# Kernel tuning notes

Hardware: AMD Instinct MI355X
Metric: run time of the kernel (lower is better)

## Reference

```python
import jax, jax.numpy as jnp
import numpy as np

EPS = 1e-5

def _conv1x1(x, w, b):
    # x: (b,c,h,w), w: (o,c) -> (b,o,h,w)
    return jnp.einsum('bchw,oc->bohw', x, w) + b[None, :, None, None]

def _maxpool2(x):
    b, c, h, w = x.shape
    return x.reshape(b, c, h // 2, 2, w // 2, 2).max(axis=(3, 5))

def setup_inputs() -> dict:
    key = jax.random.key(0)
    ks = jax.random.split(key, 11)
    C, CI, H, W, B = 256, 128, 64, 64, 8
    s = 0.05
    return {
        'x': jax.random.normal(ks[0], (B, C, H, W), jnp.float32),
        'Wg': jax.random.normal(ks[1], (CI, C), jnp.float32) * s,
        'bg': jax.random.normal(ks[2], (CI,), jnp.float32) * s,
        'Wt': jax.random.normal(ks[3], (CI, C), jnp.float32) * s,
        'bt': jax.random.normal(ks[4], (CI,), jnp.float32) * s,
        'Wp': jax.random.normal(ks[5], (CI, C), jnp.float32) * s,
        'bp': jax.random.normal(ks[6], (CI,), jnp.float32) * s,
        'Ww': jax.random.normal(ks[7], (C, CI), jnp.float32) * s,
        'bw': jax.random.normal(ks[8], (C,), jnp.float32) * s,
        'gamma': jax.random.normal(ks[9], (C,), jnp.float32),
        'beta': jax.random.normal(ks[10], (C,), jnp.float32),
    }

def reference(x, Wg, bg, Wt, bt, Wp, bp, Ww, bw, gamma, beta):
    b, C, H, W = x.shape
    CI = Wg.shape[0]
    # g and phi are sub-sampled by 2x2 max pool -> M = (H/2)*(W/2); theta keeps N = H*W
    g_x = _maxpool2(_conv1x1(x, Wg, bg)).reshape(b, CI, -1).transpose(0, 2, 1)   # (b,M,ci)
    theta_x = _conv1x1(x, Wt, bt).reshape(b, CI, -1).transpose(0, 2, 1)          # (b,N,ci)
    phi_x = _maxpool2(_conv1x1(x, Wp, bp)).reshape(b, CI, -1)                    # (b,ci,M)
    f = jnp.einsum('bnc,bcm->bnm', theta_x, phi_x)                               # (b,N,M)
    f_div_C = jax.nn.softmax(f, axis=-1)
    y = jnp.einsum('bnm,bmc->bnc', f_div_C, g_x)                                 # (b,N,ci)
    y = y.transpose(0, 2, 1).reshape(b, CI, H, W)
    # W: 1x1 conv + BatchNorm2d (training mode: batch statistics, biased var)
    wy = _conv1x1(y, Ww, bw)
    mean = wy.mean(axis=(0, 2, 3), keepdims=True)
    var = ((wy - mean) ** 2).mean(axis=(0, 2, 3), keepdims=True)
    wy = (wy - mean) * jax.lax.rsqrt(var + EPS)
    wy = wy * gamma[None, :, None, None] + beta[None, :, None, None]
    z = wy + x
    # self.avg_pool is AdaptiveMaxPool2d(1): global spatial max
    return z.max(axis=(2, 3), keepdims=True)
```

## Files before the change

### kernel.cpp

```cpp
#include <hip/hip_runtime.h>
#include <hip/hip_bf16.h>
#include <stdint.h>

using f32x4  = __attribute__((ext_vector_type(4))) float;
using bf16x8 = __attribute__((ext_vector_type(8))) short;
using short4v = __attribute__((ext_vector_type(4))) short;

#define DEVINL static __device__ __forceinline__

DEVINL short f2bf(float f) {
    union { float f; uint32_t u; } v; v.f = f;
    uint32_t r = (v.u + 0x7FFFu + ((v.u >> 16) & 1u)) >> 16;
    return (short)(uint16_t)r;
}
DEVINL float bf2f(short s) {
    union { uint32_t u; float f; } v; v.u = ((uint32_t)(uint16_t)s) << 16;
    return v.f;
}
DEVINL float fexp2(float x) {
    float r;
    asm("v_exp_f32 %0, %1" : "=v"(r) : "v"(x));
    return r;
}

DEVINL void gld16(const short* g, short* l) {
    __builtin_amdgcn_global_load_lds(
        (const __attribute__((address_space(1))) unsigned int*)g,
        (__attribute__((address_space(3))) unsigned int*)l, 16, 0, 0);
}

#define LOG2E 1.44269504f

__global__ __launch_bounds__(256) void k0_prep(
        const float* __restrict__ Wg, const float* __restrict__ Wt, const float* __restrict__ Wp,
        const float* __restrict__ bg, const float* __restrict__ bt, const float* __restrict__ bp,
        const float* __restrict__ Ww,
        short* __restrict__ W_all, short* __restrict__ Ww16, float* __restrict__ b_all) {
    int i = blockIdx.x * 256 + threadIdx.x;
    if (i < 384 * 256) {
        int r = i >> 8, c = i & 255;
        float v = (r < 128) ? Wg[r * 256 + c]
                : (r < 256) ? Wt[(r - 128) * 256 + c] * LOG2E
                            : Wp[(r - 256) * 256 + c];
        W_all[i] = f2bf(v);
    } else if (i < 384 * 256 + 256 * 128) {
        int j = i - 384 * 256;
        Ww16[j] = f2bf(Ww[j]);
    }
    if (i < 384) {
        b_all[i] = (i < 128) ? bg[i] : (i < 256) ? bt[i - 128] * LOG2E : bp[i - 256];
    }
}

__global__ __launch_bounds__(256) void k1_conv(const float* __restrict__ x,
        const short* __restrict__ W_all, const float* __restrict__ b_all,
        short* __restrict__ OutT, short* __restrict__ Kmat, short* __restrict__ Vmat) {
    __shared__ short xs[128 * 32];
    __shared__ short obuf[128 * 128];
    const int ntile = blockIdx.x;
    const int otile = blockIdx.y;
    const int b     = blockIdx.z;
    const int tid  = threadIdx.x;
    const int lane = tid & 63;
    const int wave = tid >> 6;
    const int wn = wave >> 1, wo = wave & 1;
    const int l15 = lane & 15, lh = lane >> 4;

    f32x4 acc[4][4];
    #pragma unroll
    for (int i = 0; i < 4; i++)
        #pragma unroll
        for (int j = 0; j < 4; j++) acc[i][j] = f32x4{0.f, 0.f, 0.f, 0.f};

    const int n0 = ntile * 128;
    const int ob = otile * 128 + wo * 64;
    const float* xb = x + (size_t)b * 256 * 4096;

    const int srow_base = (lane & 15) + wave * 16;
    const int sc0 = (lane >> 4) * 8;

    for (int kt = 0; kt < 8; kt++) {
        __syncthreads();
        #pragma unroll
        for (int p = 0; p < 2; p++) {
            int row = srow_base + p * 64;
            const float* xp = xb + (size_t)(kt * 32 + sc0) * 4096 + n0 + row;
            bf16x8 w8;
            #pragma unroll
            for (int j = 0; j < 8; j++) w8[j] = f2bf(xp[(size_t)j * 4096]);
            int ch = (sc0 >> 3) ^ ((row >> 1) & 3);
            *(bf16x8*)&xs[row * 32 + ch * 8] = w8;
        }
        __syncthreads();

        bf16x8 a[4], w[4];
        #pragma unroll
        for (int nf = 0; nf < 4; nf++) {
            int row = wn * 64 + nf * 16 + l15;
            int ch  = lh ^ ((row >> 1) & 3);
            a[nf] = *(const bf16x8*)&xs[row * 32 + ch * 8];
        }
        #pragma unroll
        for (int of = 0; of < 4; of++)
            w[of] = *(const bf16x8*)(W_all + (size_t)(ob + of * 16 + l15) * 256 + kt * 32 + lh * 8);
        #pragma unroll
        for (int nf = 0; nf < 4; nf++)
            #pragma unroll
            for (int of = 0; of < 4; of++)
                acc[nf][of] = __builtin_amdgcn_mfma_f32_16x16x32_bf16(a[nf], w[of], acc[nf][of], 0, 0, 0);
    }

    #pragma unroll
    for (int of = 0; of < 4; of++) {
        int ocol = wo * 64 + of * 16 + l15;
        float bias = b_all[otile * 128 + ocol];
        #pragma unroll
        for (int nf = 0; nf < 4; nf++)
            #pragma unroll
            for (int r = 0; r < 4; r++) {
                int n  = wn * 64 + nf * 16 + lh * 4 + r;
                int ch = (ocol >> 3) ^ (n & 15);
                obuf[n * 128 + ch * 8 + (ocol & 7)] = f2bf(acc[nf][of][r] + bias);
            }
    }
    __syncthreads();

    if (otile == 1) {
        #pragma unroll
        for (int p = 0; p < 8; p++) {
            int n  = wave * 4 + lh + p * 16;
            int ch = l15 ^ (n & 15);
            bf16x8 v = *(const bf16x8*)&obuf[n * 128 + ch * 8];
            *(bf16x8*)(OutT + ((size_t)b * 4096 + n0 + n) * 128 + l15 * 8) = v;
        }
    } else if (otile == 2) {
        const int wp = tid >> 3;
        const int cc = (tid & 7) * 16;
        short* kdst = Kmat + ((size_t)b * 1024 + ntile * 32 + wp) * 128 + cc;
        #pragma unroll
        for (int cblk = 0; cblk < 2; cblk++) {
            const int chunk = (cc >> 3) + cblk;
            float mx[8];
            #pragma unroll
            for (int j = 0; j < 8; j++) mx[j] = -1e30f;
            #pragma unroll
            for (int q4 = 0; q4 < 4; q4++) {
                int n = (q4 >> 1) * 64 + 2 * wp + (q4 & 1);
                bf16x8 v = *(const bf16x8*)&obuf[n * 128 + ((chunk ^ (n & 15)) * 8)];
                #pragma unroll
                for (int j = 0; j < 8; j++) mx[j] = fmaxf(mx[j], bf2f(v[j]));
            }
            bf16x8 vo;
            #pragma unroll
            for (int j = 0; j < 8; j++) vo[j] = f2bf(mx[j]);
            *(bf16x8*)(kdst + cblk * 8) = vo;
        }
    } else {
        const int c   = tid >> 1;
        const int wp0 = (tid & 1) * 16;
        const int chb = c >> 3, cl = c & 7;
        #pragma unroll
        for (int half = 0; half < 2; half++) {
            bf16x8 vo;
            #pragma unroll
            for (int j = 0; j < 8; j++) {
                int wp = wp0 + half * 8 + j;
                float mx = -1e30f;
                #pragma unroll
                for (int q4 = 0; q4 < 4; q4++) {
                    int n = (q4 >> 1) * 64 + 2 * wp + (q4 & 1);
                    mx = fmaxf(mx, bf2f(obuf[n * 128 + ((chb ^ (n & 15)) * 8) + cl]));
                }
                vo[j] = f2bf(mx);
            }
            *(bf16x8*)(Vmat + ((size_t)b * 128 + c) * 1024 + ntile * 32 + wp0 + half * 8) = vo;
        }
    }
}

__global__ __launch_bounds__(256) void k3_attn(const short* __restrict__ OutT,
        const short* __restrict__ Kmat, const short* __restrict__ Vmat,
        const short* __restrict__ Ww16, const float* __restrict__ bw,
        short* __restrict__ wy) {
    __shared__ short smem[36864];
    short* const sKb = smem;
    short* const sVb = smem + 16384;
    short* const sPb = smem + 32768;

    const int bid = blockIdx.x;
    const int b   = bid & 7;
    const int nt  = bid >> 3;
    const int tid = threadIdx.x;
    const int lane = tid & 63;
    const int wave = tid >> 6;
    const int l15 = lane & 15, lh = lane >> 4;
    const int nblk = nt * 64;
    const int n0 = nblk + wave * 16;

    const short* Kb = Kmat + (size_t)b * 1024 * 128;
    const short* Vb = Vmat + (size_t)b * 128 * 1024;
    short* sPw = sPb + wave * 1024;

    auto STAGE = [&](int t, int bufi) {
        const int m0 = t * 64;
        #pragma unroll
        for (int i = 0; i < 4; i++) {
            const int segb = (i * 4 + wave) * 64;
            const int rowK = (segb >> 4) + (lane >> 4);
            const int chkK = lane & 15;
            gld16(Kb + (size_t)(m0 + rowK) * 128 + ((chkK ^ (rowK & 15)) << 3),
                  sKb + bufi * 8192 + segb * 8);
            const int rowV = (segb >> 3) + (lane >> 3);
            const int chkV = lane & 7;
            gld16(Vb + (size_t)rowV * 1024 + m0 + ((chkV ^ (rowV & 7)) << 3),
                  sVb + bufi * 8192 + segb * 8);
        }
    };

    bf16x8 q[4];
    {
        const short* qrow = OutT + ((size_t)b * 4096 + n0 + l15) * 128;
        #pragma unroll
        for (int ks = 0; ks < 4; ks++)
            q[ks] = *(const bf16x8*)(qrow + ks * 32 + lh * 8);
    }

    f32x4 y[8];
    #pragma unroll
    for (int cf = 0; cf < 8; cf++) y[cf] = f32x4{0.f, 0.f, 0.f, 0.f};
    float mrun = -1e30f, lrun = 0.f;

    STAGE(0, 0);
    int cur = 0;

    for (int t = 0; t < 16; t++) {
        if (t < 15) {
            STAGE(t + 1, cur ^ 1);
            asm volatile("s_waitcnt vmcnt(8)" ::: "memory");
        } else {
            asm volatile("s_waitcnt vmcnt(0)" ::: "memory");
        }
        __builtin_amdgcn_s_barrier();
        __builtin_amdgcn_sched_barrier(0);

        const short* cK = sKb + cur * 8192;
        const short* cV = sVb + cur * 8192;

        f32x4 S[4];
        #pragma unroll
        for (int mf = 0; mf < 4; mf++) S[mf] = f32x4{0.f, 0.f, 0.f, 0.f};
        #pragma unroll
        for (int ks = 0; ks < 4; ks++) {
            bf16x8 kf[4];
            #pragma unroll
            for (int mf = 0; mf < 4; mf++) {
                int mrow = mf * 16 + l15;
                int jj   = ks * 4 + lh;
                kf[mf] = *(const bf16x8*)&cK[mrow * 128 + ((jj ^ (mrow & 15)) << 3)];
            }
            __builtin_amdgcn_s_setprio(1);
            #pragma unroll
            for (int mf = 0; mf < 4; mf++)
                S[mf] = __builtin_amdgcn_mfma_f32_16x16x32_bf16(kf[mf], q[ks], S[mf], 0, 0, 0);
            __builtin_amdgcn_s_setprio(0);
        }

        float pm = S[0][0];
        #pragma unroll
        for (int mf = 0; mf < 4; mf++)
            #pragma unroll
            for (int r = 0; r < 4; r++) pm = fmaxf(pm, S[mf][r]);
        pm = fmaxf(pm, __shfl_xor(pm, 16));
        pm = fmaxf(pm, __shfl_xor(pm, 32));

        if (__any(pm > mrun + 8.656f)) {
            float mnew  = fmaxf(mrun, pm);
            float alpha = fexp2(mrun - mnew);
            mrun = mnew;
            lrun *= alpha;
            float aR[4];
            #pragma unroll
            for (int r = 0; r < 4; r++) aR[r] = __shfl(alpha, lh * 4 + r);
            #pragma unroll
            for (int cf = 0; cf < 8; cf++)
                #pragma unroll
                for (int r = 0; r < 4; r++) y[cf][r] *= aR[r];
        }
        float rs = 0.f;
        #pragma unroll
        for (int mf = 0; mf < 4; mf++)
            #pragma unroll
            for (int r = 0; r < 4; r++) {
                float p = fexp2(S[mf][r] - mrun);
                S[mf][r] = p;
                rs += p;
            }
        rs += __shfl_xor(rs, 16);
        rs += __shfl_xor(rs, 32);
        lrun += rs;

        #pragma unroll
        for (int mf = 0; mf < 4; mf++) {
            short4v pk = { f2bf(S[mf][0]), f2bf(S[mf][1]), f2bf(S[mf][2]), f2bf(S[mf][3]) };
            *(short4v*)&sPw[(l15 << 6) + (((mf * 4 + lh) ^ l15) << 2)] = pk;
        }

        #pragma unroll
        for (int ks2 = 0; ks2 < 2; ks2++) {
            int u0 = ks2 * 8 + lh * 2;
            short4v lo = *(const short4v*)&sPw[(l15 << 6) + (((u0)     ^ l15) << 2)];
            short4v hi = *(const short4v*)&sPw[(l15 << 6) + (((u0 + 1) ^ l15) << 2)];
            bf16x8 pa = { lo.x, lo.y, lo.z, lo.w, hi.x, hi.y, hi.z, hi.w };
            int jj = ks2 * 4 + lh;
            __builtin_amdgcn_s_setprio(1);
            #pragma unroll
            for (int cf = 0; cf < 8; cf++) {
                int crow = cf * 16 + l15;
                bf16x8 vf = *(const bf16x8*)&cV[crow * 64 + ((jj ^ (crow & 7)) << 3)];
                y[cf] = __builtin_amdgcn_mfma_f32_16x16x32_bf16(pa, vf, y[cf], 0, 0, 0);
            }
            __builtin_amdgcn_s_setprio(0);
        }

        __builtin_amdgcn_sched_barrier(0);
        __builtin_amdgcn_s_barrier();
        cur ^= 1;
    }

    float linv[4];
    #pragma unroll
    for (int r = 0; r < 4; r++) linv[r] = 1.f / __shfl(lrun, lh * 4 + r);

    short* const Yt = smem;
    #pragma unroll
    for (int cf = 0; cf < 8; cf++) {
        int c = cf * 16 + l15;
        #pragma unroll
        for (int r = 0; r < 4; r++) {
            int n = wave * 16 + lh * 4 + r;
            Yt[n * 128 + (((c >> 3) ^ (n & 15)) << 3) + (c & 7)] = f2bf(y[cf][r] * linv[r]);
        }
    }
    __syncthreads();

    bf16x8 by[4][4];
    #pragma unroll
    for (int nf = 0; nf < 4; nf++)
        #pragma unroll
        for (int ks = 0; ks < 4; ks++) {
            int n  = nf * 16 + l15;
            int kc = ks * 4 + lh;
            by[nf][ks] = *(const bf16x8*)&Yt[n * 128 + ((kc ^ (n & 15)) << 3)];
        }

    short* const sOut = smem + 8192 + wave * 4608;
    const int obase = wave * 64;
    #pragma unroll
    for (int of = 0; of < 4; of++) {
        bf16x8 aw[4];
        #pragma unroll
        for (int ks = 0; ks < 4; ks++)
            aw[ks] = *(const bf16x8*)(Ww16 + (size_t)(obase + of * 16 + l15) * 128 + ks * 32 + lh * 8);
        #pragma unroll
        for (int nf = 0; nf < 4; nf++) {
            f32x4 acc = f32x4{0.f, 0.f, 0.f, 0.f};
            #pragma unroll
            for (int ks = 0; ks < 4; ks++)
                acc = __builtin_amdgcn_mfma_f32_16x16x32_bf16(aw[ks], by[nf][ks], acc, 0, 0, 0);
            #pragma unroll
            for (int r = 0; r < 4; r++) {
                int o_loc = of * 16 + lh * 4 + r;
                sOut[o_loc * 72 + nf * 16 + l15] = f2bf(acc[r] + bw[obase + o_loc]);
            }
        }
    }

    #pragma unroll
    for (int p = 0; p < 8; p++) {
        int o_loc = p * 8 + (lane >> 3);
        int n8    = (lane & 7) * 8;
        bf16x8 v = *(const bf16x8*)&sOut[o_loc * 72 + n8];
        *(bf16x8*)(wy + ((size_t)b * 256 + obase + o_loc) * 4096 + nblk + n8) = v;
    }
}

__global__ __launch_bounds__(256) void k4s_stats(const short* __restrict__ wy,
        float* __restrict__ stats) {
    const int o = blockIdx.x;
    const int tid = threadIdx.x;
    float s = 0.f, s2 = 0.f;
    #pragma unroll
    for (int b = 0; b < 8; b++) {
        const short* p = wy + ((size_t)b * 256 + o) * 4096;
        #pragma unroll
        for (int i = 0; i < 2; i++) {
            bf16x8 v = *(const bf16x8*)(p + (tid + i * 256) * 8);
            #pragma unroll
            for (int j = 0; j < 8; j++) {
                float f = bf2f(v[j]);
                s += f; s2 += f * f;
            }
        }
    }
    #pragma unroll
    for (int off = 1; off < 64; off <<= 1) { s += __shfl_xor(s, off); s2 += __shfl_xor(s2, off); }
    __shared__ float red[4][2];
    if ((tid & 63) == 0) { red[tid >> 6][0] = s; red[tid >> 6][1] = s2; }
    __syncthreads();
    if (tid == 0) {
        stats[o * 2]     = red[0][0] + red[1][0] + red[2][0] + red[3][0];
        stats[o * 2 + 1] = red[0][1] + red[1][1] + red[2][1] + red[3][1];
    }
}

__global__ __launch_bounds__(256) void k5_bnmax(const short* __restrict__ wy,
        const float* __restrict__ x, const float* __restrict__ stats,
        const float* __restrict__ gamma, const float* __restrict__ beta,
        float* __restrict__ outp) {
    int b = blockIdx.x >> 8;
    int o = blockIdx.x & 255;
    int tid = threadIdx.x;
    float mean = stats[o * 2] * (1.f / 32768.f);
    float var  = stats[o * 2 + 1] * (1.f / 32768.f) - mean * mean;
    float rstd = rsqrtf(var + 1e-5f);
    float A = rstd * gamma[o];
    float B = beta[o] - mean * A;
    const short* pw = wy + ((size_t)b * 256 + o) * 4096;
    const float* px = x + ((size_t)b * 256 + o) * 4096;
    float mx = -1e30f;
    #pragma unroll
    for (int j = 0; j < 2; j++) {
        int e = (tid + j * 256) * 8;
        bf16x8 w8 = *(const bf16x8*)(pw + e);
        float4 xa = *(const float4*)(px + e);
        float4 xb = *(const float4*)(px + e + 4);
        mx = fmaxf(mx, bf2f(w8[0]) * A + B + xa.x);
        mx = fmaxf(mx, bf2f(w8[1]) * A + B + xa.y);
        mx = fmaxf(mx, bf2f(w8[2]) * A + B + xa.z);
        mx = fmaxf(mx, bf2f(w8[3]) * A + B + xa.w);
        mx = fmaxf(mx, bf2f(w8[4]) * A + B + xb.x);
        mx = fmaxf(mx, bf2f(w8[5]) * A + B + xb.y);
        mx = fmaxf(mx, bf2f(w8[6]) * A + B + xb.z);
        mx = fmaxf(mx, bf2f(w8[7]) * A + B + xb.w);
    }
    #pragma unroll
    for (int off = 1; off < 64; off <<= 1) mx = fmaxf(mx, __shfl_xor(mx, off));
    __shared__ float red[4];
    if ((tid & 63) == 0) red[tid >> 6] = mx;
    __syncthreads();
    if (tid == 0)
        outp[b * 256 + o] = fmaxf(fmaxf(red[0], red[1]), fmaxf(red[2], red[3]));
}

extern "C" void kernel_launch(void* const* d_in, const int* in_sizes, int n_in,
                              void* d_out, int out_size, void* d_ws, size_t ws_size,
                              hipStream_t stream) {
    const float* x     = (const float*)d_in[0];
    const float* Wg    = (const float*)d_in[1];
    const float* bg    = (const float*)d_in[2];
    const float* Wt    = (const float*)d_in[3];
    const float* bt    = (const float*)d_in[4];
    const float* Wp    = (const float*)d_in[5];
    const float* bp    = (const float*)d_in[6];
    const float* Ww    = (const float*)d_in[7];
    const float* bw    = (const float*)d_in[8];
    const float* gamma = (const float*)d_in[9];
    const float* beta  = (const float*)d_in[10];
    float* outp = (float*)d_out;

    char* ws = (char*)d_ws;
    size_t off = 0;
    auto alloc = [&](size_t bytes) -> void* {
        void* p = ws + off;
        off = (off + bytes + 255) & ~(size_t)255;
        return p;
    };
    short* W_all = (short*)alloc((size_t)384 * 256 * 2);
    short* Ww16  = (short*)alloc((size_t)256 * 128 * 2);
    float* b_all = (float*)alloc((size_t)384 * 4);
    short* OutT  = (short*)alloc((size_t)8 * 4096 * 128 * 2);
    short* Kmat  = (short*)alloc((size_t)8 * 1024 * 128 * 2);
    short* Vmat  = (short*)alloc((size_t)8 * 128 * 1024 * 2);
    short* wy    = (short*)alloc((size_t)8 * 256 * 4096 * 2);
    float* stats = (float*)alloc((size_t)256 * 2 * 4);

    k0_prep<<<512, 256, 0, stream>>>(Wg, Wt, Wp, bg, bt, bp, Ww, W_all, Ww16, b_all);
    k1_conv<<<dim3(32, 3, 8), 256, 0, stream>>>(x, W_all, b_all, OutT, Kmat, Vmat);
    k3_attn<<<512, 256, 0, stream>>>(OutT, Kmat, Vmat, Ww16, bw, wy);
    k4s_stats<<<256, 256, 0, stream>>>(wy, stats);
    k5_bnmax<<<2048, 256, 0, stream>>>(wy, x, stats, gamma, beta, outp);
}
```

Measured before the change: 88.93 us.

## Fuse BN statistics into attention epilogue and compute softmax row sums via MFMA

```diff
diff --git a/kernel.cpp b/kernel.cpp
--- a/kernel.cpp
+++ b/kernel.cpp
@@ -22,6 +22,11 @@
     asm("v_exp_f32 %0, %1" : "=v"(r) : "v"(x));
     return r;
 }
+DEVINL uint32_t cvtpk(float a, float b) {
+    uint32_t r;
+    asm("v_cvt_pk_bf16_f32 %0, %1, %2" : "=v"(r) : "v"(a), "v"(b));
+    return r;
+}
 
 DEVINL void gld16(const short* g, short* l) {
     __builtin_amdgcn_global_load_lds(
@@ -35,8 +40,13 @@
         const float* __restrict__ Wg, const float* __restrict__ Wt, const float* __restrict__ Wp,
         const float* __restrict__ bg, const float* __restrict__ bt, const float* __restrict__ bp,
         const float* __restrict__ Ww,
-        short* __restrict__ W_all, short* __restrict__ Ww16, float* __restrict__ b_all) {
+        short* __restrict__ W_all, short* __restrict__ Ww16, float* __restrict__ b_all,
+        float* __restrict__ stats) {
     int i = blockIdx.x * 256 + threadIdx.x;
+    if (blockIdx.x == 0) {
+        stats[threadIdx.x] = 0.f;
+        stats[threadIdx.x + 256] = 0.f;
+    }
     if (i < 384 * 256) {
         int r = i >> 8, c = i & 255;
         float v = (r < 128) ? Wg[r * 256 + c]
@@ -181,7 +191,7 @@
 __global__ __launch_bounds__(256) void k3_attn(const short* __restrict__ OutT,
         const short* __restrict__ Kmat, const short* __restrict__ Vmat,
         const short* __restrict__ Ww16, const float* __restrict__ bw,
-        short* __restrict__ wy) {
+        short* __restrict__ wy, float* __restrict__ stats) {
     __shared__ short smem[36864];
     short* const sKb = smem;
     short* const sVb = smem + 16384;
@@ -224,11 +234,15 @@
         for (int ks = 0; ks < 4; ks++)
             q[ks] = *(const bf16x8*)(qrow + ks * 32 + lh * 8);
     }
+    bf16x8 vone;
+    #pragma unroll
+    for (int j = 0; j < 8; j++) vone[j] = (short)0x3F80;
 
     f32x4 y[8];
     #pragma unroll
     for (int cf = 0; cf < 8; cf++) y[cf] = f32x4{0.f, 0.f, 0.f, 0.f};
-    float mrun = -1e30f, lrun = 0.f;
+    f32x4 ysum = f32x4{0.f, 0.f, 0.f, 0.f};
+    float mrun = -1e30f;
 
     STAGE(0, 0);
     int cur = 0;
@@ -277,7 +291,6 @@
             float mnew  = fmaxf(mrun, pm);
             float alpha = fexp2(mrun - mnew);
             mrun = mnew;
-            lrun *= alpha;
             float aR[4];
             #pragma unroll
             for (int r = 0; r < 4; r++) aR[r] = __shfl(alpha, lh * 4 + r);
@@ -285,24 +298,19 @@
             for (int cf = 0; cf < 8; cf++)
                 #pragma unroll
                 for (int r = 0; r < 4; r++) y[cf][r] *= aR[r];
-        }
-        float rs = 0.f;
+            #pragma unroll
+            for (int r = 0; r < 4; r++) ysum[r] *= aR[r];
+        }
         #pragma unroll
         for (int mf = 0; mf < 4; mf++)
             #pragma unroll
-            for (int r = 0; r < 4; r++) {
-                float p = fexp2(S[mf][r] - mrun);
-                S[mf][r] = p;
-                rs += p;
-            }
-        rs += __shfl_xor(rs, 16);
-        rs += __shfl_xor(rs, 32);
-        lrun += rs;
+            for (int r = 0; r < 4; r++)
+                S[mf][r] = fexp2(S[mf][r] - mrun);
 
         #pragma unroll
         for (int mf = 0; mf < 4; mf++) {
-            short4v pk = { f2bf(S[mf][0]), f2bf(S[mf][1]), f2bf(S[mf][2]), f2bf(S[mf][3]) };
-            *(short4v*)&sPw[(l15 << 6) + (((mf * 4 + lh) ^ l15) << 2)] = pk;
+            uint2 pk = { cvtpk(S[mf][0], S[mf][1]), cvtpk(S[mf][2], S[mf][3]) };
+            *(uint2*)&sPw[(l15 << 6) + (((mf * 4 + lh) ^ l15) << 2)] = pk;
         }
 
         #pragma unroll
@@ -319,6 +327,7 @@
                 bf16x8 vf = *(const bf16x8*)&cV[crow * 64 + ((jj ^ (crow & 7)) << 3)];
                 y[cf] = __builtin_amdgcn_mfma_f32_16x16x32_bf16(pa, vf, y[cf], 0, 0, 0);
             }
+            ysum = __builtin_amdgcn_mfma_f32_16x16x32_bf16(pa, vone, ysum, 0, 0, 0);
             __builtin_amdgcn_s_setprio(0);
         }
 
@@ -329,7 +338,7 @@
 
     float linv[4];
     #pragma unroll
-    for (int r = 0; r < 4; r++) linv[r] = 1.f / __shfl(lrun, lh * 4 + r);
+    for (int r = 0; r < 4; r++) linv[r] = 1.f / ysum[r];
 
     short* const Yt = smem;
     #pragma unroll
@@ -381,35 +390,18 @@
         int n8    = (lane & 7) * 8;
         bf16x8 v = *(const bf16x8*)&sOut[o_loc * 72 + n8];
         *(bf16x8*)(wy + ((size_t)b * 256 + obase + o_loc) * 4096 + nblk + n8) = v;
-    }
-}
-
-__global__ __launch_bounds__(256) void k4s_stats(const short* __restrict__ wy,
-        float* __restrict__ stats) {
-    const int o = blockIdx.x;
-    const int tid = threadIdx.x;
-    float s = 0.f, s2 = 0.f;
-    #pragma unroll
-    for (int b = 0; b < 8; b++) {
-        const short* p = wy + ((size_t)b * 256 + o) * 4096;
-        #pragma unroll
-        for (int i = 0; i < 2; i++) {
-            bf16x8 v = *(const bf16x8*)(p + (tid + i * 256) * 8);
-            #pragma unroll
-            for (int j = 0; j < 8; j++) {
-                float f = bf2f(v[j]);
-                s += f; s2 += f * f;
-            }
-        }
-    }
-    #pragma unroll
-    for (int off = 1; off < 64; off <<= 1) { s += __shfl_xor(s, off); s2 += __shfl_xor(s2, off); }
-    __shared__ float red[4][2];
-    if ((tid & 63) == 0) { red[tid >> 6][0] = s; red[tid >> 6][1] = s2; }
-    __syncthreads();
-    if (tid == 0) {
-        stats[o * 2]     = red[0][0] + red[1][0] + red[2][0] + red[3][0];
-        stats[o * 2 + 1] = red[0][1] + red[1][1] + red[2][1] + red[3][1];
+        float s = 0.f, s2 = 0.f;
+        #pragma unroll
+        for (int j = 0; j < 8; j++) {
+            float f = bf2f(v[j]);
+            s += f; s2 += f * f;
+        }
+        #pragma unroll
+        for (int off = 1; off < 8; off <<= 1) { s += __shfl_xor(s, off); s2 += __shfl_xor(s2, off); }
+        if ((lane & 7) == 0) {
+            atomicAdd(&stats[(obase + o_loc) * 2], s);
+            atomicAdd(&stats[(obase + o_loc) * 2 + 1], s2);
+        }
     }
 }
 
@@ -484,9 +476,8 @@
     short* wy    = (short*)alloc((size_t)8 * 256 * 4096 * 2);
     float* stats = (float*)alloc((size_t)256 * 2 * 4);
 
-    k0_prep<<<512, 256, 0, stream>>>(Wg, Wt, Wp, bg, bt, bp, Ww, W_all, Ww16, b_all);
+    k0_prep<<<512, 256, 0, stream>>>(Wg, Wt, Wp, bg, bt, bp, Ww, W_all, Ww16, b_all, stats);
     k1_conv<<<dim3(32, 3, 8), 256, 0, stream>>>(x, W_all, b_all, OutT, Kmat, Vmat);
-    k3_attn<<<512, 256, 0, stream>>>(OutT, Kmat, Vmat, Ww16, bw, wy);
-    k4s_stats<<<256, 256, 0, stream>>>(wy, stats);
+    k3_attn<<<512, 256, 0, stream>>>(OutT, Kmat, Vmat, Ww16, bw, wy, stats);
     k5_bnmax<<<2048, 256, 0, stream>>>(wy, x, stats, gamma, beta, outp);
 }
```

After: 103.7 us. 16.6% more time.
